# Kernel tuning notes

Measured on AMD Instinct MI355X. Metric: run time of the kernel, lower is better.

The kernel has to match this reference:

```python
import jax, jax.numpy as jnp
import numpy as np

SIZE = 14          # feature-map side (448 image / stride 32)
IMG_STRIDE = 32    # feature->image coordinate stride
RATIOS = [(4, 4), (3, 5), (5, 3), (6, 6), (5, 7), (7, 5), (8, 8), (6, 10), (10, 6)]
GROUPS = [(0, 3), (3, 6), (6, 9)]   # ratio index ranges per scale group
N_LIST = [3, 2, 1]                   # proposals kept per group (sum = proposalN = 6)
IOU_THRESHS = [0.25, 0.25, 0.25]
WIN_NUMS = [(SIZE - h + 1) * (SIZE - w + 1) for h, w in RATIOS]  # 121,120,120,81,80,80,49,45,45
OFFS = np.cumsum([0] + WIN_NUMS)


def _make_coords():
    # image-space [x0,y0,x1,y1] per window, same order as flattened avgpool outputs
    coords = []
    for h, w in RATIOS:
        Ho, Wo = SIZE - h + 1, SIZE - w + 1
        for i in range(Ho):
            for j in range(Wo):
                x0 = i * IMG_STRIDE - 1
                y0 = j * IMG_STRIDE - 1
                x1 = x0 + h * IMG_STRIDE
                y1 = y0 + w * IMG_STRIDE
                coords.append([max(x0, 0), max(y0, 0), x1, y1])
    return np.asarray(coords, np.int32)  # [741, 4]


def setup_inputs() -> dict:
    key = jax.random.key(0)
    B = 65536
    x = jax.random.normal(key, (B, 1, SIZE, SIZE), dtype=jnp.float32)
    coords = jnp.asarray(_make_coords())
    return {"x": x, "coords": coords, "proposalN": 6}


def _avgpool_scores(x):
    # x: [B,1,H,W] -> concat of flattened VALID avgpools, [B, sum(WIN_NUMS)]
    B = x.shape[0]
    outs = []
    for h, w in RATIOS:
        s = jax.lax.reduce_window(x, 0.0, jax.lax.add, (1, 1, h, w), (1, 1, 1, 1), 'VALID')
        outs.append((s / (h * w)).reshape(B, -1))
    return jnp.concatenate(outs, axis=1)


def _nms_group(scores, coords_f, areas, N, thresh):
    # greedy NMS: repeatedly take argmax of remaining scores, suppress IoU>thresh.
    # Matches the torch/numpy loop (sorted-walk == repeated argmax for distinct scores).
    W = scores.shape[0]
    def step(carry, _):
        mask, last = carry
        any_v = jnp.any(mask)
        idx = jnp.argmax(jnp.where(mask, scores, -jnp.inf)).astype(jnp.int32)
        idx = jnp.where(any_v, idx, last)  # if exhausted, repeat last pick (as original)
        c = coords_f[idx]
        lx = jnp.minimum(coords_f[:, 2], c[2]) - jnp.maximum(coords_f[:, 0], c[0]) + 1.0
        ly = jnp.minimum(coords_f[:, 3], c[3]) - jnp.maximum(coords_f[:, 1], c[1]) + 1.0
        inter = jnp.where((lx < 0) | (ly < 0), 0.0, lx * ly)
        iou = inter / (areas + areas[idx] - inter)
        return (mask & (iou <= thresh), idx), idx
    init = (jnp.ones((W,), dtype=bool), jnp.int32(0))
    _, idxs = jax.lax.scan(step, init, None, length=N)
    return idxs  # [N] int32


def reference(x, coords, proposalN):
    all_scores = _avgpool_scores(x)                 # [B, 741]
    coords_f = coords.astype(jnp.float32)
    areas = (coords_f[:, 2] - coords_f[:, 0] + 1.0) * (coords_f[:, 3] - coords_f[:, 1] + 1.0)
    idx_parts = []
    for g, (a, b) in enumerate(GROUPS):
        s, e = int(OFFS[a]), int(OFFS[b])
        cf, ar = coords_f[s:e], areas[s:e]
        N, t = N_LIST[g], IOU_THRESHS[g]
        f = lambda sc, cf=cf, ar=ar, N=N, t=t: _nms_group(sc, cf, ar, N, t)
        idx_parts.append(jax.vmap(f)(all_scores[:, s:e]) + s)  # [B, N]
    proposalN_indices = jnp.concatenate(idx_parts, axis=1)      # [B, proposalN]
    proposalN_windows_scores = jnp.take_along_axis(all_scores, proposalN_indices, axis=1)
    window_scores = all_scores
    return proposalN_indices, proposalN_windows_scores, window_scores
```

## Files before the change

kernel.cpp:

```cpp
#include <hip/hip_runtime.h>
#include <stdint.h>
#include <math.h>

#define NW 741
#define NEG_INF_KEY 0x007FFFFFu

template<int H, int W, int OFF>
__device__ __forceinline__ void score_ratio(const float* __restrict__ im,
                                            float* __restrict__ wk,
                                            float* __restrict__ wrow,
                                            const int lane) {
  constexpr int Wo = 14 - W + 1;
  constexpr int Ho = 14 - H + 1;
  constexpr int NWIN = Ho * Wo;
  for (int o = lane; o < NWIN; o += 64) {
    const int i = o / Wo, j = o - i * Wo;
    const float* p = im + i * 14 + j;
    float acc = 0.0f;
#pragma unroll
    for (int di = 0; di < H; ++di)
#pragma unroll
      for (int dj = 0; dj < W; ++dj)
        acc += p[di * 14 + dj];
    const float sc = acc / (float)(H * W);
    wk[OFF + o] = sc;
    wrow[OFF + o] = sc;
  }
}

__global__ __launch_bounds__(256) void appm_kernel(
    const float* __restrict__ x, const int* __restrict__ coords,
    float* __restrict__ out, int B) {

  __shared__ float c_x0[NW], c_y0[NW], c_x1[NW], c_y1[NW], c_area[NW];
  __shared__ float img[4][196];
  __shared__ float work[4][NW];

  const int t = threadIdx.x;
  const int wv = t >> 6;
  const int lane = t & 63;
  const int img0 = blockIdx.x * 4;
  const int imgi = img0 + wv;
  const bool active = (imgi < B);

  for (int widx = t; widx < NW; widx += 256) {
    const int4 c = ((const int4*)coords)[widx];
    const float fx0 = (float)c.x, fy0 = (float)c.y;
    const float fx1 = (float)c.z, fy1 = (float)c.w;
    c_x0[widx] = fx0; c_y0[widx] = fy0; c_x1[widx] = fx1; c_y1[widx] = fy1;
    c_area[widx] = (fx1 - fx0 + 1.0f) * (fy1 - fy0 + 1.0f);
  }

  {
    int lim = (B - img0) * 196;
    if (lim > 784) lim = 784;
    const float* xb = x + (long long)img0 * 196;
    for (int u = t; u < lim; u += 256) ((float*)img)[u] = xb[u];
  }
  __syncthreads();

  float* wk = work[wv];
  const float* im = img[wv];
  if (active) {
    float* wrow = out + (long long)B * 12 + (long long)imgi * NW;
    score_ratio<4, 4, 0>(im, wk, wrow, lane);
    score_ratio<3, 5, 121>(im, wk, wrow, lane);
    score_ratio<5, 3, 241>(im, wk, wrow, lane);
    score_ratio<6, 6, 361>(im, wk, wrow, lane);
    score_ratio<5, 7, 442>(im, wk, wrow, lane);
    score_ratio<7, 5, 522>(im, wk, wrow, lane);
    score_ratio<8, 8, 602>(im, wk, wrow, lane);
    score_ratio<6, 10, 651>(im, wk, wrow, lane);
    score_ratio<10, 6, 696>(im, wk, wrow, lane);
  }
  __syncthreads();

  if (active) {
    float my_idx_f = 0.0f, my_score = 0.0f;
    int pick = 0;
    constexpr int gs_[3] = {0, 361, 602};
    constexpr int ge_[3] = {361, 602, 741};
    constexpr int gn_[3] = {3, 2, 1};
#pragma unroll
    for (int g = 0; g < 3; g++) {
      int last = gs_[g];
      float last_sc = 0.0f;
#pragma unroll
      for (int n = 0; n < gn_[g]; n++) {
        unsigned bkey = 0u;
        int bidx = 0;
        for (int o = gs_[g] + lane; o < ge_[g]; o += 64) {
          const unsigned u = __float_as_uint(wk[o]);
          const unsigned key = (u & 0x80000000u) ? ~u : (u | 0x80000000u);
          if (key > bkey) { bkey = key; bidx = o; }
        }
#pragma unroll
        for (int dsh = 1; dsh < 64; dsh <<= 1) {
          const unsigned okey = (unsigned)__shfl_xor((int)bkey, dsh, 64);
          const int oidx = __shfl_xor(bidx, dsh, 64);
          if (okey > bkey || (okey == bkey && oidx < bidx)) { bkey = okey; bidx = oidx; }
        }
        const bool found = (bkey > NEG_INF_KEY);
        int idx; float sc;
        if (found) {
          idx = bidx;
          const unsigned u = (bkey & 0x80000000u) ? (bkey ^ 0x80000000u) : ~bkey;
          sc = __uint_as_float(u);
        } else {
          idx = last; sc = last_sc;
        }
        last = idx; last_sc = sc;
        if (lane == pick) { my_idx_f = (float)idx; my_score = sc; }
        pick++;

        if (n + 1 < gn_[g]) {
          const float cx0 = c_x0[idx], cy0 = c_y0[idx];
          const float cx1 = c_x1[idx], cy1 = c_y1[idx];
          const float car = c_area[idx];
          for (int o = gs_[g] + lane; o < ge_[g]; o += 64) {
            const float lx = fminf(c_x1[o], cx1) - fmaxf(c_x0[o], cx0) + 1.0f;
            const float ly = fminf(c_y1[o], cy1) - fmaxf(c_y0[o], cy0) + 1.0f;
            const float inter = (lx < 0.0f || ly < 0.0f) ? 0.0f : lx * ly;
            const float iou = inter / (c_area[o] + car - inter);
            if (iou > 0.25f) wk[o] = -INFINITY;
          }
          __builtin_amdgcn_wave_barrier();
        }
      }
    }
    if (lane < 6) {
      const long long b6 = (long long)imgi * 6 + lane;
      out[b6] = my_idx_f;
      out[(long long)B * 6 + b6] = my_score;
    }
  }
}

extern "C" void kernel_launch(void* const* d_in, const int* in_sizes, int n_in,
                              void* d_out, int out_size, void* d_ws, size_t ws_size,
                              hipStream_t stream) {
  const float* x = (const float*)d_in[0];
  const int* coords = (const int*)d_in[1];
  float* out = (float*)d_out;
  const int B = in_sizes[0] / 196;
  const int nblk = (B + 3) / 4;
  appm_kernel<<<dim3(nblk), dim3(256), 0, stream>>>(x, coords, out, B);
}
```

Measured before the change: 456.7 us.

## Process two images per wavefront with interleaved pooling, DPP argmax, packed boxes

Each wavefront now handles two images: their pixels are interleaved in shared memory so each pooling loop reads float2, and both images share the box-coordinate loads during NMS suppression. The cross-lane argmax switches from shuffle-xor to DPP row operations plus readlane. Scores are stored as pre-converted sortable keys, suppression compares against 4*inter instead of dividing, and the block-wide barrier after scoring becomes a wave barrier. This amortises address math and coordinate loads over two images and halves the grid. The cost is more registers and LDS per block, which may lower occupancy.

```diff
diff --git a/kernel.cpp b/kernel.cpp
--- a/kernel.cpp
+++ b/kernel.cpp
@@ -5,26 +5,57 @@
 #define NW 741
 #define NEG_INF_KEY 0x007FFFFFu
 
+__device__ __forceinline__ unsigned score_key(float f) {
+  const unsigned u = __float_as_uint(f);
+  return (u & 0x80000000u) ? ~u : (u | 0x80000000u);
+}
+__device__ __forceinline__ float key_score(unsigned k) {
+  return __uint_as_float((k & 0x80000000u) ? (k ^ 0x80000000u) : ~k);
+}
+
+template<int CTRL>
+__device__ __forceinline__ void argmax_step(unsigned& k, int& i) {
+  const unsigned tk = (unsigned)__builtin_amdgcn_update_dpp(0, (int)k, CTRL, 0xF, 0xF, true);
+  const int ti = __builtin_amdgcn_update_dpp(0, i, CTRL, 0xF, 0xF, true);
+  if (tk > k || (tk == k && ti < i)) { k = tk; i = ti; }
+}
+__device__ __forceinline__ void wave_argmax(unsigned& k, int& i) {
+  argmax_step<0x111>(k, i);
+  argmax_step<0x112>(k, i);
+  argmax_step<0x114>(k, i);
+  argmax_step<0x118>(k, i);
+  argmax_step<0x142>(k, i);
+  argmax_step<0x143>(k, i);
+  k = (unsigned)__builtin_amdgcn_readlane((int)k, 63);
+  i = __builtin_amdgcn_readlane(i, 63);
+}
+
 template<int H, int W, int OFF>
-__device__ __forceinline__ void score_ratio(const float* __restrict__ im,
-                                            float* __restrict__ wk,
-                                            float* __restrict__ wrow,
-                                            const int lane) {
+__device__ __forceinline__ void score_ratio2(const float2* __restrict__ im2,
+                                             unsigned* __restrict__ wk2,
+                                             float* __restrict__ wrowA,
+                                             float* __restrict__ wrowB,
+                                             const int lane, const bool hasB) {
   constexpr int Wo = 14 - W + 1;
   constexpr int Ho = 14 - H + 1;
   constexpr int NWIN = Ho * Wo;
   for (int o = lane; o < NWIN; o += 64) {
     const int i = o / Wo, j = o - i * Wo;
-    const float* p = im + i * 14 + j;
-    float acc = 0.0f;
+    const float2* p = im2 + (i * 14 + j);
+    float2 acc; acc.x = 0.0f; acc.y = 0.0f;
 #pragma unroll
     for (int di = 0; di < H; ++di)
 #pragma unroll
-      for (int dj = 0; dj < W; ++dj)
-        acc += p[di * 14 + dj];
-    const float sc = acc / (float)(H * W);
-    wk[OFF + o] = sc;
-    wrow[OFF + o] = sc;
+      for (int dj = 0; dj < W; ++dj) {
+        const float2 v = p[di * 14 + dj];
+        acc.x += v.x; acc.y += v.y;
+      }
+    const float scA = acc.x / (float)(H * W);
+    const float scB = acc.y / (float)(H * W);
+    wrowA[OFF + o] = scA;
+    if (hasB) wrowB[OFF + o] = scB;
+    uint2 kk; kk.x = score_key(scA); kk.y = score_key(scB);
+    *(uint2*)&wk2[(OFF + o) * 2] = kk;
   }
 }
 
@@ -32,106 +63,121 @@
     const float* __restrict__ x, const int* __restrict__ coords,
     float* __restrict__ out, int B) {
 
-  __shared__ float c_x0[NW], c_y0[NW], c_x1[NW], c_y1[NW], c_area[NW];
-  __shared__ float img[4][196];
-  __shared__ float work[4][NW];
+  __shared__ float4 c_box[NW];
+  __shared__ float c_ar[NW];
+  __shared__ float imgp[4][392];
+  __shared__ unsigned wkk[4][NW * 2];
 
   const int t = threadIdx.x;
   const int wv = t >> 6;
   const int lane = t & 63;
-  const int img0 = blockIdx.x * 4;
-  const int imgi = img0 + wv;
-  const bool active = (imgi < B);
+  const int img0 = blockIdx.x * 8;
+  const int imgA = img0 + wv * 2;
+  const int imgB = imgA + 1;
+  const bool hasA = (imgA < B);
+  const bool hasB = (imgB < B);
 
-  for (int widx = t; widx < NW; widx += 256) {
-    const int4 c = ((const int4*)coords)[widx];
+  for (int w = t; w < NW; w += 256) {
+    const int4 c = ((const int4*)coords)[w];
     const float fx0 = (float)c.x, fy0 = (float)c.y;
     const float fx1 = (float)c.z, fy1 = (float)c.w;
-    c_x0[widx] = fx0; c_y0[widx] = fy0; c_x1[widx] = fx1; c_y1[widx] = fy1;
-    c_area[widx] = (fx1 - fx0 + 1.0f) * (fy1 - fy0 + 1.0f);
+    c_box[w] = make_float4(fx0, fy0, fx1, fy1);
+    c_ar[w] = (fx1 - fx0 + 1.0f) * (fy1 - fy0 + 1.0f);
   }
 
   {
-    int lim = (B - img0) * 196;
-    if (lim > 784) lim = 784;
+    int nimg = B - img0; if (nimg > 8) nimg = 8;
+    const int lim = nimg * 196;
     const float* xb = x + (long long)img0 * 196;
-    for (int u = t; u < lim; u += 256) ((float*)img)[u] = xb[u];
+    for (int u = t; u < lim; u += 256) {
+      const int i = u / 196, k = u - i * 196;
+      imgp[i >> 1][k * 2 + (i & 1)] = xb[u];
+    }
   }
   __syncthreads();
 
-  float* wk = work[wv];
-  const float* im = img[wv];
-  if (active) {
-    float* wrow = out + (long long)B * 12 + (long long)imgi * NW;
-    score_ratio<4, 4, 0>(im, wk, wrow, lane);
-    score_ratio<3, 5, 121>(im, wk, wrow, lane);
-    score_ratio<5, 3, 241>(im, wk, wrow, lane);
-    score_ratio<6, 6, 361>(im, wk, wrow, lane);
-    score_ratio<5, 7, 442>(im, wk, wrow, lane);
-    score_ratio<7, 5, 522>(im, wk, wrow, lane);
-    score_ratio<8, 8, 602>(im, wk, wrow, lane);
-    score_ratio<6, 10, 651>(im, wk, wrow, lane);
-    score_ratio<10, 6, 696>(im, wk, wrow, lane);
-  }
-  __syncthreads();
+  if (hasA) {
+    const float2* im2 = (const float2*)imgp[wv];
+    unsigned* wk2 = wkk[wv];
+    float* wrowA = out + (long long)B * 12 + (long long)imgA * NW;
+    float* wrowB = wrowA + NW;
 
-  if (active) {
-    float my_idx_f = 0.0f, my_score = 0.0f;
+    score_ratio2<4, 4, 0>(im2, wk2, wrowA, wrowB, lane, hasB);
+    score_ratio2<3, 5, 121>(im2, wk2, wrowA, wrowB, lane, hasB);
+    score_ratio2<5, 3, 241>(im2, wk2, wrowA, wrowB, lane, hasB);
+    score_ratio2<6, 6, 361>(im2, wk2, wrowA, wrowB, lane, hasB);
+    score_ratio2<5, 7, 442>(im2, wk2, wrowA, wrowB, lane, hasB);
+    score_ratio2<7, 5, 522>(im2, wk2, wrowA, wrowB, lane, hasB);
+    score_ratio2<8, 8, 602>(im2, wk2, wrowA, wrowB, lane, hasB);
+    score_ratio2<6, 10, 651>(im2, wk2, wrowA, wrowB, lane, hasB);
+    score_ratio2<10, 6, 696>(im2, wk2, wrowA, wrowB, lane, hasB);
+    __builtin_amdgcn_wave_barrier();
+
+    float myIA = 0.0f, mySA = 0.0f, myIB = 0.0f, mySB = 0.0f;
     int pick = 0;
     constexpr int gs_[3] = {0, 361, 602};
     constexpr int ge_[3] = {361, 602, 741};
     constexpr int gn_[3] = {3, 2, 1};
 #pragma unroll
     for (int g = 0; g < 3; g++) {
-      int last = gs_[g];
-      float last_sc = 0.0f;
+      const int gs = gs_[g], ge = ge_[g];
+      int lastA = gs, lastB = gs;
+      float lastSA = 0.0f, lastSB = 0.0f;
 #pragma unroll
       for (int n = 0; n < gn_[g]; n++) {
-        unsigned bkey = 0u;
-        int bidx = 0;
-        for (int o = gs_[g] + lane; o < ge_[g]; o += 64) {
-          const unsigned u = __float_as_uint(wk[o]);
-          const unsigned key = (u & 0x80000000u) ? ~u : (u | 0x80000000u);
-          if (key > bkey) { bkey = key; bidx = o; }
+        unsigned bkA = 0u, bkB = 0u;
+        int biA = 0, biB = 0;
+        for (int o = gs + lane; o < ge; o += 64) {
+          const uint2 kk = *(const uint2*)&wkk[wv][o * 2];
+          if (kk.x > bkA) { bkA = kk.x; biA = o; }
+          if (kk.y > bkB) { bkB = kk.y; biB = o; }
         }
-#pragma unroll
-        for (int dsh = 1; dsh < 64; dsh <<= 1) {
-          const unsigned okey = (unsigned)__shfl_xor((int)bkey, dsh, 64);
-          const int oidx = __shfl_xor(bidx, dsh, 64);
-          if (okey > bkey || (okey == bkey && oidx < bidx)) { bkey = okey; bidx = oidx; }
-        }
-        const bool found = (bkey > NEG_INF_KEY);
-        int idx; float sc;
-        if (found) {
-          idx = bidx;
-          const unsigned u = (bkey & 0x80000000u) ? (bkey ^ 0x80000000u) : ~bkey;
-          sc = __uint_as_float(u);
-        } else {
-          idx = last; sc = last_sc;
-        }
-        last = idx; last_sc = sc;
-        if (lane == pick) { my_idx_f = (float)idx; my_score = sc; }
+        wave_argmax(bkA, biA);
+        wave_argmax(bkB, biB);
+
+        int idxA, idxB; float scA, scB;
+        if (bkA > NEG_INF_KEY) { idxA = biA; scA = key_score(bkA); }
+        else { idxA = lastA; scA = lastSA; }
+        if (bkB > NEG_INF_KEY) { idxB = biB; scB = key_score(bkB); }
+        else { idxB = lastB; scB = lastSB; }
+        lastA = idxA; lastSA = scA;
+        lastB = idxB; lastSB = scB;
+        if (lane == pick) { myIA = (float)idxA; mySA = scA; myIB = (float)idxB; mySB = scB; }
         pick++;
 
         if (n + 1 < gn_[g]) {
-          const float cx0 = c_x0[idx], cy0 = c_y0[idx];
-          const float cx1 = c_x1[idx], cy1 = c_y1[idx];
-          const float car = c_area[idx];
-          for (int o = gs_[g] + lane; o < ge_[g]; o += 64) {
-            const float lx = fminf(c_x1[o], cx1) - fmaxf(c_x0[o], cx0) + 1.0f;
-            const float ly = fminf(c_y1[o], cy1) - fmaxf(c_y0[o], cy0) + 1.0f;
-            const float inter = (lx < 0.0f || ly < 0.0f) ? 0.0f : lx * ly;
-            const float iou = inter / (c_area[o] + car - inter);
-            if (iou > 0.25f) wk[o] = -INFINITY;
+          const float4 bA = c_box[idxA]; const float aA = c_ar[idxA];
+          const float4 bB = c_box[idxB]; const float aB = c_ar[idxB];
+          for (int o = gs + lane; o < ge; o += 64) {
+            const float4 cb = c_box[o];
+            const float ar = c_ar[o];
+            const float lxA = fminf(cb.z, bA.z) - fmaxf(cb.x, bA.x) + 1.0f;
+            const float lyA = fminf(cb.w, bA.w) - fmaxf(cb.y, bA.y) + 1.0f;
+            const float inA = (lxA < 0.0f || lyA < 0.0f) ? 0.0f : lxA * lyA;
+            const bool supA = (4.0f * inA > ar + aA - inA);
+            const float lxB = fminf(cb.z, bB.z) - fmaxf(cb.x, bB.x) + 1.0f;
+            const float lyB = fminf(cb.w, bB.w) - fmaxf(cb.y, bB.y) + 1.0f;
+            const float inB = (lxB < 0.0f || lyB < 0.0f) ? 0.0f : lxB * lyB;
+            const bool supB = (4.0f * inB > ar + aB - inB);
+            uint2 kk = *(uint2*)&wkk[wv][o * 2];
+            if (supA) kk.x = 0u;
+            if (supB) kk.y = 0u;
+            *(uint2*)&wkk[wv][o * 2] = kk;
           }
           __builtin_amdgcn_wave_barrier();
         }
       }
     }
+
     if (lane < 6) {
-      const long long b6 = (long long)imgi * 6 + lane;
-      out[b6] = my_idx_f;
-      out[(long long)B * 6 + b6] = my_score;
+      const long long a6 = (long long)imgA * 6 + lane;
+      out[a6] = myIA;
+      out[(long long)B * 6 + a6] = mySA;
+      if (hasB) {
+        const long long b6 = (long long)imgB * 6 + lane;
+        out[b6] = myIB;
+        out[(long long)B * 6 + b6] = mySB;
+      }
     }
   }
 }
@@ -143,6 +189,6 @@
   const int* coords = (const int*)d_in[1];
   float* out = (float*)d_out;
   const int B = in_sizes[0] / 196;
-  const int nblk = (B + 3) / 4;
+  const int nblk = (B + 7) / 8;
   appm_kernel<<<dim3(nblk), dim3(256), 0, stream>>>(x, coords, out, B);
 }
```

Measured after the change: 443.4 us. -2.9%, faster.
